# Kernel tuning notes

Measured on AMD Instinct MI355X. Metric: run time of the kernel, lower is better.

The kernel has to match this reference:

```python
import jax, jax.numpy as jnp
import numpy as np

N, NF, DIM, H, DH, DEPTH, EDIM, NB = 256, 127, 128, 8, 64, 6, 3, 512
INNER = H * DH  # 512
SCALE = DH ** -0.5
EPS = 1e-5


def setup_inputs() -> dict:
    key = jax.random.key(0)
    ks = jax.random.split(key, 16)
    p = lambda k, shape: jax.random.normal(k, shape, jnp.float32) * 0.02
    return {
        "coordinates": jax.random.normal(ks[0], (N, 3), jnp.float32),
        "bonds": jax.random.randint(ks[1], (NB, 2), 0, N),
        "noise_level": jax.random.uniform(ks[2], (1,), jnp.float32),
        "atom_emb": p(ks[3], (N, NF)),
        "ln1_g": jnp.ones((DEPTH, DIM)), "ln1_b": jnp.zeros((DEPTH, DIM)),
        "Wq": p(ks[4], (DEPTH, DIM, INNER)), "bq": jnp.zeros((DEPTH, INNER)),
        "Wkv": p(ks[5], (DEPTH, DIM, 2 * INNER)), "bkv": jnp.zeros((DEPTH, 2 * INNER)),
        "We": p(ks[6], (DEPTH, EDIM, INNER)), "be": jnp.zeros((DEPTH, INNER)),
        "Wo": p(ks[7], (DEPTH, INNER, DIM)), "bo": jnp.zeros((DEPTH, DIM)),
        "Wg1": p(ks[8], (DEPTH, 3 * DIM)),
        "ln2_g": jnp.ones((DEPTH, DIM)), "ln2_b": jnp.zeros((DEPTH, DIM)),
        "W1": p(ks[9], (DEPTH, DIM, 4 * DIM)), "b1": jnp.zeros((DEPTH, 4 * DIM)),
        "W2": p(ks[10], (DEPTH, 4 * DIM, DIM)), "b2": jnp.zeros((DEPTH, DIM)),
        "Wg2": p(ks[11], (DEPTH, 3 * DIM)),
        "out_w": p(ks[12], (DIM, 1)), "out_b": jnp.zeros((1,)),
    }


def _layernorm(x, g, b):
    m = jnp.mean(x, axis=-1, keepdims=True)
    v = jnp.mean((x - m) ** 2, axis=-1, keepdims=True)
    return (x - m) * jax.lax.rsqrt(v + EPS) * g + b


def _gated_residual(x, res, Wg):
    # Linear(3*dim -> 1, no bias) then sigmoid; mask is all-True so no masking.
    gate = jax.nn.sigmoid(jnp.concatenate([x, res, x - res], axis=-1) @ Wg)[..., None]
    return x * gate + res * (1.0 - gate)


def _forward(coordinates, bonds, noise_level, atom_emb, ln1_g, ln1_b, Wq, bq,
             Wkv, bkv, We, be, Wo, bo, Wg1, ln2_g, ln2_b, W1, b1, W2, b2, Wg2,
             out_w, out_b):
    n = coordinates.shape[0]
    # nodes: [n, NF] atom embeddings (looked up at arange(n)) + noise column -> [n, DIM]
    noise_col = jnp.broadcast_to(noise_level.reshape(1, 1), (n, 1))
    nodes = jnp.concatenate([atom_emb, noise_col], axis=-1)
    # dense edge tensor [n, n, 3]: coordinate differences at bonded pairs, antisymmetric
    bi, bj = bonds[:, 0], bonds[:, 1]
    diff = coordinates[bi] - coordinates[bj]
    edges = jnp.zeros((n, n, EDIM), jnp.float32).at[bi, bj].set(diff).at[bj, bi].set(-diff)

    for l in range(DEPTH):
        # --- edge-biased multi-head attention (PreNorm) ---
        x = _layernorm(nodes, ln1_g[l], ln1_b[l])
        q = (x @ Wq[l] + bq[l]).reshape(n, H, DH).transpose(1, 0, 2)          # [h, i, d]
        kv = x @ Wkv[l] + bkv[l]
        k = kv[:, :INNER].reshape(n, H, DH).transpose(1, 0, 2)                # [h, j, d]
        v = kv[:, INNER:].reshape(n, H, DH).transpose(1, 0, 2)                # [h, j, d]
        e = (edges @ We[l] + be[l]).reshape(n, n, H, DH).transpose(2, 0, 1, 3)  # [h, i, j, d]
        k_ij = k[:, None, :, :] + e                                            # [h, i, j, d]
        v_ij = v[:, None, :, :] + e
        sim = jnp.einsum('hid,hijd->hij', q, k_ij) * SCALE
        attn = jax.nn.softmax(sim, axis=-1)  # mask is all ones -> no-op
        out = jnp.einsum('hij,hijd->hid', attn, v_ij)                          # [h, i, d]
        out = out.transpose(1, 0, 2).reshape(n, INNER) @ Wo[l] + bo[l]         # [n, DIM]
        nodes = _gated_residual(out, nodes, Wg1[l])
        # --- feedforward (PreNorm) + gated residual ---
        y = _layernorm(nodes, ln2_g[l], ln2_b[l])
        y = jax.nn.gelu(y @ W1[l] + b1[l], approximate=False) @ W2[l] + b2[l]
        nodes = _gated_residual(y, nodes, Wg2[l])

    energy = nodes @ out_w + out_b  # [n, 1]
    return energy[None, :, :]       # [1, n, 1]


def reference(coordinates, bonds, noise_level, atom_emb, ln1_g, ln1_b, Wq, bq,
              Wkv, bkv, We, be, Wo, bo, Wg1, ln2_g, ln2_b, W1, b1, W2, b2, Wg2,
              out_w, out_b):
    return _forward(coordinates, bonds, noise_level, atom_emb, ln1_g, ln1_b,
                    Wq, bq, Wkv, bkv, We, be, Wo, bo, Wg1, ln2_g, ln2_b,
                    W1, b1, W2, b2, Wg2, out_w, out_b)
```

## Files before the change

### kernel.cpp

```cpp
#include <hip/hip_runtime.h>

#define NN     256
#define NF     127
#define DIM    128
#define NH     8
#define DH     64
#define INNER  512
#define DEPTH  6
#define NB     512
#define ATTN_SCALE 0.125f
#define LN_EPS 1e-5f

typedef _Float16 f16;
union H8 { uint4 u; f16 h[8]; };

#define FMA4(A_, S_, V_) { A_.x=fmaf(S_,(V_).x,A_.x); A_.y=fmaf(S_,(V_).y,A_.y); \
                           A_.z=fmaf(S_,(V_).z,A_.z); A_.w=fmaf(S_,(V_).w,A_.w); }

__device__ __forceinline__ float wred_sum(float v){
#pragma unroll
  for(int o=32;o;o>>=1) v += __shfl_xor(v,o);
  return v;
}
__device__ __forceinline__ float wred_max(float v){
#pragma unroll
  for(int o=32;o;o>>=1) v = fmaxf(v,__shfl_xor(v,o));
  return v;
}
__device__ __forceinline__ float2 wred_sum2(float a, float b){
#pragma unroll
  for(int o=32;o;o>>=1){ a += __shfl_xor(a,o); b += __shfl_xor(b,o); }
  return make_float2(a,b);
}

__device__ __forceinline__ void ln_wave(float n0, float n1,
                                        const float* g, const float* b, int l,
                                        float& x0, float& x1){
  float2 sv = wred_sum2(n0+n1, n0*n0+n1*n1);
  float m  = sv.x*(1.f/DIM);
  float var = sv.y*(1.f/DIM) - m*m;
  float rs = rsqrtf(var + LN_EPS);
  x0 = (n0-m)*rs*g[l]    + b[l];
  x1 = (n1-m)*rs*g[64+l] + b[64+l];
}

__device__ __forceinline__ void gate_wave(float o0, float o1, float& n0, float& n1,
                                          const float* Wg, int l){
  float gv = o0*Wg[l]    + n0*Wg[DIM+l]    + (o0-n0)*Wg[2*DIM+l]
           + o1*Wg[64+l] + n1*Wg[DIM+64+l] + (o1-n1)*Wg[2*DIM+64+l];
  gv = wred_sum(gv);
  float gate = 1.f/(1.f + expf(-gv));
  n0 = o0*gate + n0*(1.f-gate);
  n1 = o1*gate + n1*(1.f-gate);
}

__device__ __forceinline__ void mvp128_512h(const float* __restrict__ xin,
                                            const f16* __restrict__ W,
                                            float* __restrict__ SC, int t){
  const int cg8 = (t&63)<<3, fg = t>>6, f0 = fg<<4;
  const f16* __restrict__ p = W + f0*INNER + cg8;
  float4 a0 = make_float4(0.f,0.f,0.f,0.f), a1 = a0;
#pragma unroll
  for(int k=0;k<16;k++){
    H8 wv; wv.u = *(const uint4*)(p + k*INNER);
    float x = xin[f0+k];
    a0.x=fmaf(x,(float)wv.h[0],a0.x); a0.y=fmaf(x,(float)wv.h[1],a0.y);
    a0.z=fmaf(x,(float)wv.h[2],a0.z); a0.w=fmaf(x,(float)wv.h[3],a0.w);
    a1.x=fmaf(x,(float)wv.h[4],a1.x); a1.y=fmaf(x,(float)wv.h[5],a1.y);
    a1.z=fmaf(x,(float)wv.h[6],a1.z); a1.w=fmaf(x,(float)wv.h[7],a1.w);
  }
  *(float4*)(SC + fg*INNER + cg8)     = a0;
  *(float4*)(SC + fg*INNER + cg8 + 4) = a1;
}
__device__ __forceinline__ void mvp512_128h(const float* __restrict__ ain,
                                            const f16* __restrict__ W,
                                            float* __restrict__ SC, int t){
  const int cg8 = (t&15)<<3, fg = t>>4, f0 = fg<<4;
  const f16* __restrict__ p = W + f0*DIM + cg8;
  float4 a0 = make_float4(0.f,0.f,0.f,0.f), a1 = a0;
#pragma unroll
  for(int k=0;k<16;k++){
    H8 wv; wv.u = *(const uint4*)(p + k*DIM);
    float x = ain[f0+k];
    a0.x=fmaf(x,(float)wv.h[0],a0.x); a0.y=fmaf(x,(float)wv.h[1],a0.y);
    a0.z=fmaf(x,(float)wv.h[2],a0.z); a0.w=fmaf(x,(float)wv.h[3],a0.w);
    a1.x=fmaf(x,(float)wv.h[4],a1.x); a1.y=fmaf(x,(float)wv.h[5],a1.y);
    a1.z=fmaf(x,(float)wv.h[6],a1.z); a1.w=fmaf(x,(float)wv.h[7],a1.w);
  }
  *(float4*)(SC + fg*DIM + cg8)     = a0;
  *(float4*)(SC + fg*DIM + cg8 + 4) = a1;
}
__device__ __forceinline__ void mvp128_1024(const float* __restrict__ xin,
                                            const float* __restrict__ W,
                                            float* __restrict__ SC, int t){
  const int cg4 = (t&255)<<2, rh = t>>8;
  float4 acc = make_float4(0.f,0.f,0.f,0.f);
#pragma unroll 8
  for(int f=rh*64; f<rh*64+64; f++){
    float4 wv = *(const float4*)(W + f*(2*INNER) + cg4);
    float xv = xin[f];
    FMA4(acc, xv, wv);
  }
  *(float4*)(SC + rh*(2*INNER) + cg4) = acc;
}

__device__ __forceinline__ void qkv_tail(const float* __restrict__ xs, int i,
    const f16* __restrict__ Wqh, const float* __restrict__ bq,
    const float* __restrict__ Wkv, const float* __restrict__ bkv,
    const float* __restrict__ be, float* qgn, float* kTn, float* vgn,
    float* __restrict__ SC, int t){
  mvp128_512h(xs, Wqh, SC,        t);
  mvp128_1024(xs, Wkv, SC + 4096, t);
  __syncthreads();
  {
    float s = bq[t];
#pragma unroll
    for(int fg=0; fg<8; fg++) s += SC[fg*INNER + t];
    qgn[i*INNER + t] = s;
  }
#pragma unroll
  for(int cc=0; cc<2; cc++){
    int c = t + cc*512;
    float sv = bkv[c] + SC[4096 + c] + SC[4096 + 1024 + c];
    if(c < INNER) kTn[c*NN + i]            = sv + be[c];
    else          vgn[i*INNER + c - INNER] = sv + be[c-INNER];
  }
}

__global__ __launch_bounds__(512) void k_prep(
    const float* __restrict__ Wq, const float* __restrict__ Wo,
    const float* __restrict__ W1, const float* __restrict__ W2,
    f16* Wqh, f16* Woh, f16* W1h, f16* W2h)
{
  const int NQ = DEPTH*DIM*INNER;
  const int NTOT = 4*NQ;
  for(int k = blockIdx.x*512 + threadIdx.x; k < NTOT; k += gridDim.x*512){
    float v; f16* dst;
    if(k < NQ)        { v = Wq[k];        dst = Wqh + k; }
    else if(k < 2*NQ) { v = Wo[k-NQ];     dst = Woh + (k-NQ); }
    else if(k < 3*NQ) { v = W1[k-2*NQ];   dst = W1h + (k-2*NQ); }
    else              { v = W2[k-3*NQ];   dst = W2h + (k-3*NQ); }
    *dst = (f16)v;
  }
}

__global__ __launch_bounds__(512) void k_qkv0(const float* atom_emb, const float* noise,
    float* nodes, const float* ln1_g, const float* ln1_b,
    const f16* Wqh, const float* bq, const float* Wkv, const float* bkv, const float* be,
    float* qg, float* kT, float* vg,
    const int* bonds, const float* coords, float* ebg){
  __shared__ __align__(16) float SC[6144];
  __shared__ __align__(16) float xsm[DIM];
  __shared__ __align__(16) float ebs[8*768];
  const int t = threadIdx.x, bid = blockIdx.x;
  if(bid >= NN){
    const int i0 = (bid-NN)<<3;
#pragma unroll
    for(int cc=0; cc<12; cc++) ebs[cc*512 + t] = 0.f;
    __syncthreads();
    {
      const int bi = bonds[2*t], bj = bonds[2*t+1];
      const bool hi = (bi>=i0 && bi<i0+8), hj = (bj>=i0 && bj<i0+8);
      if(hi || hj){
        float dx = coords[3*bi+0] - coords[3*bj+0];
        float dy = coords[3*bi+1] - coords[3*bj+1];
        float dz = coords[3*bi+2] - coords[3*bj+2];
        if(hi){ float* e = ebs + (bi-i0)*768; e[bj]=dx;  e[256+bj]=dy;  e[512+bj]=dz;  }
        if(hj){ float* e = ebs + (bj-i0)*768; e[bi]=-dx; e[256+bi]=-dy; e[512+bi]=-dz; }
      }
    }
    __syncthreads();
#pragma unroll
    for(int cc=0; cc<12; cc++) ebg[(size_t)i0*768 + cc*512 + t] = ebs[cc*512 + t];
    return;
  }
  const int i = bid, w = t>>6, l = t&63;
  float nd0 = (l<NF)?    atom_emb[i*NF + l]      : noise[0];
  float nd1 = (64+l<NF)? atom_emb[i*NF + 64 + l] : noise[0];
  if(w==0){ nodes[i*DIM + l] = nd0; nodes[i*DIM + 64 + l] = nd1; }
  float x0, x1;
  ln_wave(nd0, nd1, ln1_g, ln1_b, l, x0, x1);
  xsm[l] = x0; xsm[64+l] = x1;
  __syncthreads();
  qkv_tail(xsm, i, Wqh, bq, Wkv, bkv, be, qg, kT, vg, SC, t);
}

__global__ __launch_bounds__(512) void k_attn(
    const float* __restrict__ qg, const float* __restrict__ kT,
    const float* __restrict__ vg, const float* __restrict__ ebg,
    const float* __restrict__ We, float* __restrict__ aog,
    const f16* __restrict__ pfA, const f16* __restrict__ pfB,
    const f16* __restrict__ pfC, const f16* __restrict__ pfD,
    const float* __restrict__ pfE, int pf_next)
{
  __shared__ __align__(16) float qsm[8*DH];
  __shared__ __align__(16) float aW[8][NN];
  const int t = threadIdx.x;
  const int h = blockIdx.x >> 5, i0 = (blockIdx.x & 31) << 3;
  const int w = t>>6, l = t&63;
  const int qb = h*DH, j0 = l<<2;

  qsm[w*DH + l] = qg[(i0+w)*INNER + qb + l];

  {
    const int s = blockIdx.x >> 3;
    unsigned keep = 0u;
    if(t < 256){
      keep ^= ((const uint4*)((const char*)pfA + (size_t)s*4096))[t].x;
      keep ^= ((const uint4*)((const char*)pfB + (size_t)s*4096))[t].y;
      keep ^= ((const uint4*)((const char*)pfC + (size_t)s*4096))[t].z;
      if(pf_next)
        keep ^= ((const uint4*)((const char*)pfD + (size_t)s*4096))[t].w;
    }
    if(pf_next){
      keep ^= ((const uint4*)((const char*)pfE + (size_t)s*16384))[t].x;
      keep ^= ((const uint4*)((const char*)pfE + (size_t)s*16384))[512 + t].x;
    }
    asm volatile("" :: "v"(keep));
  }
  __syncthreads();

  float qwe0, qwe1, qwe2;
  {
    float qv = qsm[w*DH + l];
    qwe0 = qv*We[0*INNER + qb + l];
    qwe1 = qv*We[1*INNER + qb + l];
    qwe2 = qv*We[2*INNER + qb + l];
#pragma unroll
    for(int o=32;o;o>>=1){
      qwe0 += __shfl_xor(qwe0,o); qwe1 += __shfl_xor(qwe1,o); qwe2 += __shfl_xor(qwe2,o);
    }
  }
  const float* __restrict__ kTh = kT + qb*NN;
  float s0=0.f,s1=0.f,s2=0.f,s3=0.f;
#pragma unroll 8
  for(int o=0;o<DH;o++){
    float qv = qsm[w*DH + o];
    float4 kk = *(const float4*)(kTh + o*NN + j0);
    s0=fmaf(qv,kk.x,s0); s1=fmaf(qv,kk.y,s1); s2=fmaf(qv,kk.z,s2); s3=fmaf(qv,kk.w,s3);
  }
  const float* __restrict__ e = ebg + (size_t)(i0+w)*768;
  float4 ex = *(const float4*)(e + j0);
  float4 ey = *(const float4*)(e + 256 + j0);
  float4 ez = *(const float4*)(e + 512 + j0);
  s0 = (s0 + qwe0*ex.x + qwe1*ey.x + qwe2*ez.x)*ATTN_SCALE;
  s1 = (s1 + qwe0*ex.y + qwe1*ey.y + qwe2*ez.y)*ATTN_SCALE;
  s2 = (s2 + qwe0*ex.z + qwe1*ey.z + qwe2*ez.z)*ATTN_SCALE;
  s3 = (s3 + qwe0*ex.w + qwe1*ey.w + qwe2*ez.w)*ATTN_SCALE;
  float mx = wred_max(fmaxf(fmaxf(s0,s1),fmaxf(s2,s3)));
  float p0=expf(s0-mx), p1=expf(s1-mx), p2=expf(s2-mx), p3=expf(s3-mx);
  float inv = 1.f / wred_sum(p0+p1+p2+p3);
  float a0=p0*inv, a1=p1*inv, a2=p2*inv, a3=p3*inv;
  *(float4*)(aW[w] + j0) = make_float4(a0,a1,a2,a3);
  float c0 = a0*ex.x + a1*ex.y + a2*ex.z + a3*ex.w;
  float c1 = a0*ey.x + a1*ey.y + a2*ey.z + a3*ey.w;
  float c2 = a0*ez.x + a1*ez.y + a2*ez.z + a3*ez.w;
  c0 = wred_sum(c0); c1 = wred_sum(c1); c2 = wred_sum(c2);
  __builtin_amdgcn_wave_barrier();
  const int dq = (l&15)<<2, jg = l>>4;
  const float* __restrict__ vb = vg + qb + dq;
  float4 acc = make_float4(0.f,0.f,0.f,0.f);
#pragma unroll 8
  for(int jj=0;jj<64;jj++){
    int j = (jg<<6) + ((jj + (jg<<3)) & 63);
    float a = aW[w][j];
    float4 vv = *(const float4*)(vb + j*INNER);
    FMA4(acc, a, vv);
  }
#pragma unroll
  for(int o=16;o<64;o<<=1){
    acc.x += __shfl_xor(acc.x,o); acc.y += __shfl_xor(acc.y,o);
    acc.z += __shfl_xor(acc.z,o); acc.w += __shfl_xor(acc.w,o);
  }
  if(l<16){
    float4 we0 = *(const float4*)(We + 0*INNER + qb + dq);
    float4 we1 = *(const float4*)(We + 1*INNER + qb + dq);
    float4 we2 = *(const float4*)(We + 2*INNER + qb + dq);
    float4 ov;
    ov.x = acc.x + c0*we0.x + c1*we1.x + c2*we2.x;
    ov.y = acc.y + c0*we0.y + c1*we1.y + c2*we2.y;
    ov.z = acc.z + c0*we0.z + c1*we1.z + c2*we2.z;
    ov.w = acc.w + c0*we0.w + c1*we1.w + c2*we2.w;
    *(float4*)(aog + (i0+w)*INNER + qb + dq) = ov;
  }
}

__global__ __launch_bounds__(512) void k_layer(
    float* nodes, const float* __restrict__ aog,
    float* qg_n, float* kT_n, float* vg_n,
    const f16* __restrict__ Woh, const float* __restrict__ bo,
    const float* __restrict__ Wg1,
    const float* __restrict__ ln2_g, const float* __restrict__ ln2_b,
    const f16* __restrict__ W1h, const float* __restrict__ b1,
    const f16* __restrict__ W2h, const float* __restrict__ b2,
    const float* __restrict__ Wg2,
    const float* __restrict__ ln1_g_n, const float* __restrict__ ln1_b_n,
    const f16* __restrict__ Wqh_n, const float* __restrict__ bq_n,
    const float* __restrict__ Wkv_n, const float* __restrict__ bkv_n,
    const float* __restrict__ be_n,
    const float* __restrict__ out_w, const float* __restrict__ out_b,
    float* eout, int has_next)
{
  __shared__ __align__(16) float SC[6144];
  __shared__ __align__(16) float qs[INNER];
  __shared__ __align__(16) float aos[INNER];
  __shared__ __align__(16) float xsm[DIM];
  const int t = threadIdx.x, i = blockIdx.x;
  const int w = t>>6, l = t&63;

  aos[t] = aog[i*INNER + t];
  float nd0 = nodes[i*DIM + l];
  float nd1 = nodes[i*DIM + 64 + l];
  __syncthreads();

  mvp512_128h(aos, Woh, SC, t);
  __syncthreads();
  {
    float o0 = bo[l], o1 = bo[64+l];
#pragma unroll
    for(int fg=0; fg<32; fg++){ o0 += SC[fg*DIM + l]; o1 += SC[fg*DIM + 64 + l]; }
    gate_wave(o0, o1, nd0, nd1, Wg1, l);
    float x0, x1;
    ln_wave(nd0, nd1, ln2_g, ln2_b, l, x0, x1);
    xsm[l] = x0; xsm[64+l] = x1;
  }
  __syncthreads();

  mvp128_512h(xsm, W1h, SC, t);
  __syncthreads();
  {
    float a = b1[t];
#pragma unroll
    for(int fg=0; fg<8; fg++) a += SC[fg*INNER + t];
    qs[t] = 0.5f*a*(1.f + erff(a*0.70710678118654752440f));
  }
  __syncthreads();
  mvp512_128h(qs, W2h, SC, t);
  __syncthreads();
  {
    float y0 = b2[l], y1 = b2[64+l];
#pragma unroll
    for(int fg=0; fg<32; fg++){ y0 += SC[fg*DIM + l]; y1 += SC[fg*DIM + 64 + l]; }
    gate_wave(y0, y1, nd0, nd1, Wg2, l);
    if(w==0){ nodes[i*DIM + l] = nd0; nodes[i*DIM + 64 + l] = nd1; }
    if(has_next){
      float x0, x1;
      ln_wave(nd0, nd1, ln1_g_n, ln1_b_n, l, x0, x1);
      xsm[l] = x0; xsm[64+l] = x1;
    } else if(w==0){
      float ev = nd0*out_w[l] + nd1*out_w[64+l];
      ev = wred_sum(ev);
      if(l==0) eout[i] = ev + out_b[0];
    }
  }
  if(has_next){
    __syncthreads();
    qkv_tail(xsm, i, Wqh_n, bq_n, Wkv_n, bkv_n, be_n,
             qg_n, kT_n, vg_n, SC, t);
  }
}

extern "C" void kernel_launch(void* const* d_in, const int* in_sizes, int n_in,
                              void* d_out, int out_size, void* d_ws, size_t ws_size,
                              hipStream_t stream){
  const float* coords   = (const float*)d_in[0];
  const int*   bonds    = (const int*  )d_in[1];
  const float* noise    = (const float*)d_in[2];
  const float* atom_emb = (const float*)d_in[3];
  const float* ln1_g = (const float*)d_in[4];
  const float* ln1_b = (const float*)d_in[5];
  const float* Wq    = (const float*)d_in[6];
  const float* bq    = (const float*)d_in[7];
  const float* Wkv   = (const float*)d_in[8];
  const float* bkv   = (const float*)d_in[9];
  const float* We    = (const float*)d_in[10];
  const float* be    = (const float*)d_in[11];
  const float* Wo    = (const float*)d_in[12];
  const float* bo    = (const float*)d_in[13];
  const float* Wg1   = (const float*)d_in[14];
  const float* ln2_g = (const float*)d_in[15];
  const float* ln2_b = (const float*)d_in[16];
  const float* W1    = (const float*)d_in[17];
  const float* b1    = (const float*)d_in[18];
  const float* W2    = (const float*)d_in[19];
  const float* b2    = (const float*)d_in[20];
  const float* Wg2   = (const float*)d_in[21];
  const float* out_w = (const float*)d_in[22];
  const float* out_b = (const float*)d_in[23];

  char* base = (char*)d_ws;
  float* nodes = (float*)(base);
  float* qb0   = (float*)(base + 131072);
  float* qb1   = (float*)(base + 655360);
  float* aog   = (float*)(base + 1179648);
  float* ebg   = (float*)(base + 1703936);
  float* kb0   = (float*)(base + 2490368);
  float* kb1   = (float*)(base + 3014656);
  float* vb0   = (float*)(base + 3538944);
  float* vb1   = (float*)(base + 4063232);
  f16*   Wqh   = (f16*  )(base + 4587520);
  f16*   Woh   = (f16*  )(base + 5373952);
  f16*   W1h   = (f16*  )(base + 6160384);
  f16*   W2h   = (f16*  )(base + 6946816);
  float* eout  = (float*)d_out;

  k_prep<<<512, 512, 0, stream>>>(Wq, Wo, W1, W2, Wqh, Woh, W1h, W2h);
  k_qkv0<<<NN+32, 512, 0, stream>>>(atom_emb, noise, nodes, ln1_g, ln1_b,
                                    Wqh, bq, Wkv, bkv, be,
                                    qb0, kb0, vb0,
                                    bonds, coords, ebg);
  for(int l=0; l<DEPTH; l++){
    int has_next = (l < DEPTH-1);
    int ln = has_next ? l+1 : l;
    float* qcur = (l&1)? qb1:qb0;  float* kcur = (l&1)? kb1:kb0;  float* vcur = (l&1)? vb1:vb0;
    float* qnxt = (l&1)? qb0:qb1;  float* knxt = (l&1)? kb0:kb1;  float* vnxt = (l&1)? vb0:vb1;
    const f16* Woh_l  = Woh + (size_t)l*INNER*DIM;
    const f16* W1h_l  = W1h + (size_t)l*DIM*4*DIM;
    const f16* W2h_l  = W2h + (size_t)l*4*DIM*DIM;
    const f16* Wqh_n  = Wqh + (size_t)ln*DIM*INNER;
    const float* Wkv_n = Wkv + (size_t)ln*DIM*2*INNER;
    k_attn<<<NN, 512, 0, stream>>>(
      qcur, kcur, vcur, ebg,
      We + (size_t)l*3*INNER, aog,
      Woh_l, W1h_l, W2h_l, Wqh_n, Wkv_n, has_next);
    k_layer<<<NN, 512, 0, stream>>>(
      nodes, aog,
      qnxt, knxt, vnxt,
      Woh_l, bo + (size_t)l*DIM, Wg1 + (size_t)l*3*DIM,
      ln2_g + (size_t)l*DIM, ln2_b + (size_t)l*DIM,
      W1h_l, b1 + (size_t)l*4*DIM,
      W2h_l, b2 + (size_t)l*DIM, Wg2 + (size_t)l*3*DIM,
      ln1_g + (size_t)ln*DIM, ln1_b + (size_t)ln*DIM,
      Wqh_n, bq + (size_t)ln*INNER,
      Wkv_n, bkv + (size_t)ln*2*INNER,
      be  + (size_t)ln*INNER,
      out_w, out_b, eout, has_next);
  }
}
```

Baseline: 286.5 us.

## Stream k_layer weights through triple-buffered LDS with async global_load_lds

Rewrites the per-row layer kernel so that all weight matrices (Wo, W1, W2, next-layer Wq and Wkv) are streamed as 32KB chunks into a three-slot LDS ring using global_load_lds. Each chunk's loads are issued two steps ahead and gated by explicit vmcnt waits and barriers, so weight fetch overlaps the FMA work. Bias, layernorm and gate parameters are preloaded into a shared parameter block. This raises LDS use to well over 100KB per block, which limits occupancy, and it depends on hand-written waitcnt sequencing being correct.

```diff
diff --git a/kernel.cpp b/kernel.cpp
--- a/kernel.cpp
+++ b/kernel.cpp
@@ -12,7 +12,9 @@
 #define LN_EPS 1e-5f
 
 typedef _Float16 f16;
+typedef unsigned int u32;
 union H8 { uint4 u; f16 h[8]; };
+union H4 { uint2 u; f16 h[4]; };
 
 #define FMA4(A_, S_, V_) { A_.x=fmaf(S_,(V_).x,A_.x); A_.y=fmaf(S_,(V_).y,A_.y); \
                            A_.z=fmaf(S_,(V_).z,A_.z); A_.w=fmaf(S_,(V_).w,A_.w); }
@@ -71,24 +73,6 @@
   }
   *(float4*)(SC + fg*INNER + cg8)     = a0;
   *(float4*)(SC + fg*INNER + cg8 + 4) = a1;
-}
-__device__ __forceinline__ void mvp512_128h(const float* __restrict__ ain,
-                                            const f16* __restrict__ W,
-                                            float* __restrict__ SC, int t){
-  const int cg8 = (t&15)<<3, fg = t>>4, f0 = fg<<4;
-  const f16* __restrict__ p = W + f0*DIM + cg8;
-  float4 a0 = make_float4(0.f,0.f,0.f,0.f), a1 = a0;
-#pragma unroll
-  for(int k=0;k<16;k++){
-    H8 wv; wv.u = *(const uint4*)(p + k*DIM);
-    float x = ain[f0+k];
-    a0.x=fmaf(x,(float)wv.h[0],a0.x); a0.y=fmaf(x,(float)wv.h[1],a0.y);
-    a0.z=fmaf(x,(float)wv.h[2],a0.z); a0.w=fmaf(x,(float)wv.h[3],a0.w);
-    a1.x=fmaf(x,(float)wv.h[4],a1.x); a1.y=fmaf(x,(float)wv.h[5],a1.y);
-    a1.z=fmaf(x,(float)wv.h[6],a1.z); a1.w=fmaf(x,(float)wv.h[7],a1.w);
-  }
-  *(float4*)(SC + fg*DIM + cg8)     = a0;
-  *(float4*)(SC + fg*DIM + cg8 + 4) = a1;
 }
 __device__ __forceinline__ void mvp128_1024(const float* __restrict__ xin,
                                             const float* __restrict__ W,
@@ -104,7 +88,7 @@
   *(float4*)(SC + rh*(2*INNER) + cg4) = acc;
 }
 
-__device__ __forceinline__ void qkv_tail(const float* __restrict__ xs, int i,
+__device__ __forceinline__ void qkv_tail0(const float* __restrict__ xs, int i,
     const f16* __restrict__ Wqh, const float* __restrict__ bq,
     const float* __restrict__ Wkv, const float* __restrict__ bkv,
     const float* __restrict__ be, float* qgn, float* kTn, float* vgn,
@@ -126,6 +110,81 @@
     else          vgn[i*INNER + c - INNER] = sv + be[c-INNER];
   }
 }
+
+__device__ __forceinline__ void gld16(const float* g, float* l){
+  __builtin_amdgcn_global_load_lds(
+      (const __attribute__((address_space(1))) u32*)g,
+      (__attribute__((address_space(3))) u32*)l,
+      16, 0, 0);
+}
+__device__ __forceinline__ void stage32k(const float* __restrict__ g,
+                                         float* stg, int t){
+  const int w = t>>6, l = t&63;
+#pragma unroll
+  for(int r=0;r<4;r++){
+    const int q = (r<<3) + w;
+    gld16(g + q*256 + (l<<2), stg + q*256);
+  }
+}
+
+__device__ __forceinline__ const float* csrc(int k,
+    const float* pWo, const float* pW1, const float* pW2,
+    const float* pWq, const float* pWkv){
+  if(k < 4)  return pWo  + k*8192;
+  if(k < 8)  return pW1  + (k-4)*8192;
+  if(k < 12) return pW2  + (k-8)*8192;
+  if(k < 16) return pWq  + (k-12)*8192;
+  return pWkv + (k-16)*8192;
+}
+
+__device__ __forceinline__ void cA(const float* ch, const float* xin, int xoff,
+                                   int w, int l, float4& a0, float4& a1){
+  const f16* chh = (const f16*)ch;
+  const int r = l>>4, c8 = (l&15)<<3;
+#pragma unroll
+  for(int p=0;p<4;p++){
+    int row = p*32 + w*4 + r;
+    H8 wv; wv.u = *(const uint4*)(chh + row*128 + c8);
+    float x = xin[xoff + row];
+    a0.x=fmaf(x,(float)wv.h[0],a0.x); a0.y=fmaf(x,(float)wv.h[1],a0.y);
+    a0.z=fmaf(x,(float)wv.h[2],a0.z); a0.w=fmaf(x,(float)wv.h[3],a0.w);
+    a1.x=fmaf(x,(float)wv.h[4],a1.x); a1.y=fmaf(x,(float)wv.h[5],a1.y);
+    a1.z=fmaf(x,(float)wv.h[6],a1.z); a1.w=fmaf(x,(float)wv.h[7],a1.w);
+  }
+}
+__device__ __forceinline__ void cB(const float* ch, const float* xin, int xoff,
+                                   int w, int t, float4& a0, float4& a1){
+  const f16* chh = (const f16*)ch;
+  const int cg8 = (t&63)<<3;
+#pragma unroll
+  for(int r4=0;r4<4;r4++){
+    int row = w*4 + r4;
+    H8 wv; wv.u = *(const uint4*)(chh + row*512 + cg8);
+    float x = xin[xoff + row];
+    a0.x=fmaf(x,(float)wv.h[0],a0.x); a0.y=fmaf(x,(float)wv.h[1],a0.y);
+    a0.z=fmaf(x,(float)wv.h[2],a0.z); a0.w=fmaf(x,(float)wv.h[3],a0.w);
+    a1.x=fmaf(x,(float)wv.h[4],a1.x); a1.y=fmaf(x,(float)wv.h[5],a1.y);
+    a1.z=fmaf(x,(float)wv.h[6],a1.z); a1.w=fmaf(x,(float)wv.h[7],a1.w);
+  }
+}
+__device__ __forceinline__ void cC(const float* ch, const float* xin, int xoff,
+                                   int t, float4& acc){
+  const int cg4 = (t&255)<<2, fh = t>>8;
+#pragma unroll
+  for(int r4=0;r4<4;r4++){
+    int row = fh*4 + r4;
+    float4 wv = *(const float4*)(ch + row*1024 + cg4);
+    float x = xin[xoff + row];
+    FMA4(acc, x, wv);
+  }
+}
+
+#define KWAIT(kk, NCH_) \
+  if((kk) < (NCH_)-1) asm volatile("s_waitcnt vmcnt(4) lgkmcnt(0)" ::: "memory"); \
+  else                asm volatile("s_waitcnt vmcnt(0) lgkmcnt(0)" ::: "memory"); \
+  __builtin_amdgcn_sched_barrier(0); \
+  __builtin_amdgcn_s_barrier(); \
+  __builtin_amdgcn_sched_barrier(0);
 
 __global__ __launch_bounds__(512) void k_prep(
     const float* __restrict__ Wq, const float* __restrict__ Wo,
@@ -182,7 +241,7 @@
   ln_wave(nd0, nd1, ln1_g, ln1_b, l, x0, x1);
   xsm[l] = x0; xsm[64+l] = x1;
   __syncthreads();
-  qkv_tail(xsm, i, Wqh, bq, Wkv, bkv, be, qg, kT, vg, SC, t);
+  qkv_tail0(xsm, i, Wqh, bq, Wkv, bkv, be, qg, kT, vg, SC, t);
 }
 
 __global__ __launch_bounds__(512) void k_attn(
@@ -201,7 +260,6 @@
   const int qb = h*DH, j0 = l<<2;
 
   qsm[w*DH + l] = qg[(i0+w)*INNER + qb + l];
-
   {
     const int s = blockIdx.x >> 3;
     unsigned keep = 0u;
@@ -301,62 +359,164 @@
     const float* __restrict__ out_w, const float* __restrict__ out_b,
     float* eout, int has_next)
 {
+  __shared__ __align__(16) float stg[3*8192];
   __shared__ __align__(16) float SC[6144];
+  __shared__ __align__(16) float PRM[4352];
+  __shared__ __align__(16) float aos[INNER];
   __shared__ __align__(16) float qs[INNER];
-  __shared__ __align__(16) float aos[INNER];
   __shared__ __align__(16) float xsm[DIM];
   const int t = threadIdx.x, i = blockIdx.x;
   const int w = t>>6, l = t&63;
 
   aos[t] = aog[i*INNER + t];
-  float nd0 = nodes[i*DIM + l];
-  float nd1 = nodes[i*DIM + 64 + l];
-  __syncthreads();
-
-  mvp512_128h(aos, Woh, SC, t);
-  __syncthreads();
+  PRM[128+t]  = b1[t];
+  PRM[2048+t] = bq_n[t];
+  PRM[2560+t] = bkv_n[t];
+  PRM[3072+t] = bkv_n[512+t];
+  PRM[3584+t] = be_n[t];
+  if(t<128){
+    PRM[t]       = bo[t];
+    PRM[640+t]   = b2[t];
+    PRM[1536+t]  = ln2_g[t];
+    PRM[1664+t]  = ln2_b[t];
+    PRM[1792+t]  = ln1_g_n[t];
+    PRM[1920+t]  = ln1_b_n[t];
+    PRM[4096+t]  = out_w[t];
+    PRM[4224+t]  = nodes[i*DIM + t];
+  }
+  if(t<384){
+    PRM[768+t]  = Wg1[t];
+    PRM[1152+t] = Wg2[t];
+  }
+  asm volatile("s_waitcnt vmcnt(0) lgkmcnt(0)" ::: "memory");
+  __builtin_amdgcn_s_barrier();
+
+  const float* pWo  = (const float*)Woh;
+  const float* pW1  = (const float*)W1h;
+  const float* pW2  = (const float*)W2h;
+  const float* pWq  = (const float*)Wqh_n;
+  const float* pWkv = Wkv_n;
+  const int NCH = has_next ? 32 : 12;
+
+  stage32k(csrc(0,pWo,pW1,pW2,pWq,pWkv), stg,         t);
+  stage32k(csrc(1,pWo,pW1,pW2,pWq,pWkv), stg + 8192,  t);
+
+  float nd0 = PRM[4224+l], nd1 = PRM[4224+64+l];
+  float4 a0 = make_float4(0.f,0.f,0.f,0.f), a1 = a0;
+
+#pragma unroll
+  for(int k=0;k<4;k++){
+    KWAIT(k,NCH);
+    if(k+2 < NCH) stage32k(csrc(k+2,pWo,pW1,pW2,pWq,pWkv), stg + ((k+2)%3)*8192, t);
+    cA(stg + (k%3)*8192, aos, k*128, w, l, a0, a1);
+  }
+  { const int fg = w*4 + (l>>4), c8 = (l&15)<<3;
+    *(float4*)(SC + fg*128 + c8)     = a0;
+    *(float4*)(SC + fg*128 + c8 + 4) = a1; }
+  asm volatile("s_waitcnt lgkmcnt(0)" ::: "memory");
+  __builtin_amdgcn_sched_barrier(0);
+  __builtin_amdgcn_s_barrier();
   {
-    float o0 = bo[l], o1 = bo[64+l];
+    float o0 = PRM[l], o1 = PRM[64+l];
 #pragma unroll
     for(int fg=0; fg<32; fg++){ o0 += SC[fg*DIM + l]; o1 += SC[fg*DIM + 64 + l]; }
-    gate_wave(o0, o1, nd0, nd1, Wg1, l);
+    gate_wave(o0, o1, nd0, nd1, PRM+768, l);
     float x0, x1;
-    ln_wave(nd0, nd1, ln2_g, ln2_b, l, x0, x1);
+    ln_wave(nd0, nd1, PRM+1536, PRM+1664, l, x0, x1);
     xsm[l] = x0; xsm[64+l] = x1;
   }
-  __syncthreads();
-
-  mvp128_512h(xsm, W1h, SC, t);
-  __syncthreads();
+
+  a0 = make_float4(0.f,0.f,0.f,0.f); a1 = a0;
+#pragma unroll
+  for(int k=4;k<8;k++){
+    KWAIT(k,NCH);
+    if(k+2 < NCH) stage32k(csrc(k+2,pWo,pW1,pW2,pWq,pWkv), stg + ((k+2)%3)*8192, t);
+    cB(stg + (k%3)*8192, xsm, (k-4)*32, w, t, a0, a1);
+  }
+  { const int cg8 = (t&63)<<3;
+    *(float4*)(SC + w*512 + cg8)     = a0;
+    *(float4*)(SC + w*512 + cg8 + 4) = a1; }
+  asm volatile("s_waitcnt lgkmcnt(0)" ::: "memory");
+  __builtin_amdgcn_sched_barrier(0);
+  __builtin_amdgcn_s_barrier();
   {
-    float a = b1[t];
+    float a = PRM[128+t];
 #pragma unroll
     for(int fg=0; fg<8; fg++) a += SC[fg*INNER + t];
     qs[t] = 0.5f*a*(1.f + erff(a*0.70710678118654752440f));
   }
-  __syncthreads();
-  mvp512_128h(qs, W2h, SC, t);
-  __syncthreads();
+
+  a0 = make_float4(0.f,0.f,0.f,0.f); a1 = a0;
+#pragma unroll
+  for(int k=8;k<12;k++){
+    KWAIT(k,NCH);
+    if(k+2 < NCH) stage32k(csrc(k+2,pWo,pW1,pW2,pWq,pWkv), stg + ((k+2)%3)*8192, t);
+    cA(stg + (k%3)*8192, qs, (k-8)*128, w, l, a0, a1);
+  }
+  { const int fg = w*4 + (l>>4), c8 = (l&15)<<3;
+    *(float4*)(SC + fg*128 + c8)     = a0;
+    *(float4*)(SC + fg*128 + c8 + 4) = a1; }
+  asm volatile("s_waitcnt lgkmcnt(0)" ::: "memory");
+  __builtin_amdgcn_sched_barrier(0);
+  __builtin_amdgcn_s_barrier();
   {
-    float y0 = b2[l], y1 = b2[64+l];
+    float y0 = PRM[640+l], y1 = PRM[640+64+l];
 #pragma unroll
     for(int fg=0; fg<32; fg++){ y0 += SC[fg*DIM + l]; y1 += SC[fg*DIM + 64 + l]; }
-    gate_wave(y0, y1, nd0, nd1, Wg2, l);
-    if(w==0){ nodes[i*DIM + l] = nd0; nodes[i*DIM + 64 + l] = nd1; }
+    gate_wave(y0, y1, nd0, nd1, PRM+1152, l);
     if(has_next){
       float x0, x1;
-      ln_wave(nd0, nd1, ln1_g_n, ln1_b_n, l, x0, x1);
+      ln_wave(nd0, nd1, PRM+1792, PRM+1920, l, x0, x1);
       xsm[l] = x0; xsm[64+l] = x1;
-    } else if(w==0){
-      float ev = nd0*out_w[l] + nd1*out_w[64+l];
+    }
+  }
+
+  if(has_next){
+    a0 = make_float4(0.f,0.f,0.f,0.f); a1 = a0;
+#pragma unroll
+    for(int k=12;k<16;k++){
+      KWAIT(k,32);
+      if(k+2 < 32) stage32k(csrc(k+2,pWo,pW1,pW2,pWq,pWkv), stg + ((k+2)%3)*8192, t);
+      cB(stg + (k%3)*8192, xsm, (k-12)*32, w, t, a0, a1);
+    }
+    { const int cg8 = (t&63)<<3;
+      *(float4*)(SC + w*512 + cg8)     = a0;
+      *(float4*)(SC + w*512 + cg8 + 4) = a1; }
+
+    float4 ckv = make_float4(0.f,0.f,0.f,0.f);
+#pragma unroll
+    for(int k=16;k<32;k++){
+      KWAIT(k,32);
+      if(k+2 < 32) stage32k(csrc(k+2,pWo,pW1,pW2,pWq,pWkv), stg + ((k+2)%3)*8192, t);
+      cC(stg + (k%3)*8192, xsm, (k-16)*8, t, ckv);
+    }
+    { const int cg4 = (t&255)<<2, fh = t>>8;
+      *(float4*)(SC + 4096 + fh*1024 + cg4) = ckv; }
+    asm volatile("s_waitcnt lgkmcnt(0)" ::: "memory");
+    __builtin_amdgcn_sched_barrier(0);
+    __builtin_amdgcn_s_barrier();
+
+    {
+      float s = PRM[2048+t];
+#pragma unroll
+      for(int fg=0; fg<8; fg++) s += SC[fg*INNER + t];
+      qg_n[i*INNER + t] = s;
+    }
+#pragma unroll
+    for(int cc=0; cc<2; cc++){
+      int c = t + cc*512;
+      float sv = PRM[2560+c] + SC[4096 + c] + SC[4096 + 1024 + c];
+      if(c < INNER) kT_n[c*NN + i]            = sv + PRM[3584+c];
+      else          vg_n[i*INNER + c - INNER] = sv + PRM[3584+c-512];
+    }
+    if(w==0){ nodes[i*DIM + l] = nd0; nodes[i*DIM + 64 + l] = nd1; }
+  } else {
+    if(w==0){
+      nodes[i*DIM + l] = nd0; nodes[i*DIM + 64 + l] = nd1;
+      float ev = nd0*PRM[4096+l] + nd1*PRM[4096+64+l];
       ev = wred_sum(ev);
       if(l==0) eout[i] = ev + out_b[0];
     }
-  }
-  if(has_next){
-    __syncthreads();
-    qkv_tail(xsm, i, Wqh_n, bq_n, Wkv_n, bkv_n, be_n,
-             qg_n, kT_n, vg_n, SC, t);
   }
 }
 
```

New measurement: 307.4 us. 7.3% more time.

## Stage per-head K and V tiles in LDS for attention kernel

Applied to the files above, without the earlier changes.

The attention kernel now copies the head's transposed K slice and V slice (256x64 floats each) into shared memory once per block. The score and weighted-sum loops then read from LDS instead of having every wave re-read K and V from global/L2. The PV product is restructured so each lane owns one output dimension and loops over all 256 keys, which removes the cross-lane shuffle reduction. The roughly 138KB of shared memory limits occupancy to one block per CU. It also adds an upfront copy of 128KB per block before any compute starts.

```diff
diff --git a/kernel.cpp b/kernel.cpp
--- a/kernel.cpp
+++ b/kernel.cpp
@@ -193,13 +193,29 @@
     const f16* __restrict__ pfC, const f16* __restrict__ pfD,
     const float* __restrict__ pfE, int pf_next)
 {
+  __shared__ __align__(16) float kTs[64*NN];
+  __shared__ __align__(16) float vs[NN*64];
+  __shared__ __align__(16) float aW[8][NN];
   __shared__ __align__(16) float qsm[8*DH];
-  __shared__ __align__(16) float aW[8][NN];
   const int t = threadIdx.x;
   const int h = blockIdx.x >> 5, i0 = (blockIdx.x & 31) << 3;
   const int w = t>>6, l = t&63;
   const int qb = h*DH, j0 = l<<2;
 
+  {
+    const float* kbase = kT + qb*NN;
+#pragma unroll
+    for(int r=0;r<8;r++){
+      int idx = r*2048 + (t<<2);
+      *(float4*)(kTs + idx) = *(const float4*)(kbase + idx);
+    }
+    const int jr = t>>4, c4 = (t&15)<<2;
+#pragma unroll
+    for(int p=0;p<8;p++){
+      int j = p*32 + jr;
+      *(float4*)(vs + j*64 + c4) = *(const float4*)(vg + j*INNER + qb + c4);
+    }
+  }
   qsm[w*DH + l] = qg[(i0+w)*INNER + qb + l];
 
   {
@@ -231,12 +247,11 @@
       qwe0 += __shfl_xor(qwe0,o); qwe1 += __shfl_xor(qwe1,o); qwe2 += __shfl_xor(qwe2,o);
     }
   }
-  const float* __restrict__ kTh = kT + qb*NN;
   float s0=0.f,s1=0.f,s2=0.f,s3=0.f;
 #pragma unroll 8
   for(int o=0;o<DH;o++){
     float qv = qsm[w*DH + o];
-    float4 kk = *(const float4*)(kTh + o*NN + j0);
+    float4 kk = *(const float4*)(kTs + o*NN + j0);
     s0=fmaf(qv,kk.x,s0); s1=fmaf(qv,kk.y,s1); s2=fmaf(qv,kk.z,s2); s3=fmaf(qv,kk.w,s3);
   }
   const float* __restrict__ e = ebg + (size_t)(i0+w)*768;
@@ -257,32 +272,18 @@
   float c2 = a0*ez.x + a1*ez.y + a2*ez.z + a3*ez.w;
   c0 = wred_sum(c0); c1 = wred_sum(c1); c2 = wred_sum(c2);
   __builtin_amdgcn_wave_barrier();
-  const int dq = (l&15)<<2, jg = l>>4;
-  const float* __restrict__ vb = vg + qb + dq;
-  float4 acc = make_float4(0.f,0.f,0.f,0.f);
+  const float* aww = aW[w];
+  float acc0 = 0.f, acc1 = 0.f;
 #pragma unroll 8
-  for(int jj=0;jj<64;jj++){
-    int j = (jg<<6) + ((jj + (jg<<3)) & 63);
-    float a = aW[w][j];
-    float4 vv = *(const float4*)(vb + j*INNER);
-    FMA4(acc, a, vv);
-  }
-#pragma unroll
-  for(int o=16;o<64;o<<=1){
-    acc.x += __shfl_xor(acc.x,o); acc.y += __shfl_xor(acc.y,o);
-    acc.z += __shfl_xor(acc.z,o); acc.w += __shfl_xor(acc.w,o);
-  }
-  if(l<16){
-    float4 we0 = *(const float4*)(We + 0*INNER + qb + dq);
-    float4 we1 = *(const float4*)(We + 1*INNER + qb + dq);
-    float4 we2 = *(const float4*)(We + 2*INNER + qb + dq);
-    float4 ov;
-    ov.x = acc.x + c0*we0.x + c1*we1.x + c2*we2.x;
-    ov.y = acc.y + c0*we0.y + c1*we1.y + c2*we2.y;
-    ov.z = acc.z + c0*we0.z + c1*we1.z + c2*we2.z;
-    ov.w = acc.w + c0*we0.w + c1*we1.w + c2*we2.w;
-    *(float4*)(aog + (i0+w)*INNER + qb + dq) = ov;
-  }
+  for(int j=0;j<NN;j+=2){
+    acc0 = fmaf(aww[j],   vs[j*64 + l],     acc0);
+    acc1 = fmaf(aww[j+1], vs[(j+1)*64 + l], acc1);
+  }
+  float ov = acc0 + acc1
+           + c0*We[0*INNER + qb + l]
+           + c1*We[1*INNER + qb + l]
+           + c2*We[2*INNER + qb + l];
+  aog[(i0+w)*INNER + qb + l] = ov;
 }
 
 __global__ __launch_bounds__(512) void k_layer(
```

Result: faster. 269.8 us (-5.8%).
